# Kernel tuning notes

Hardware: AMD Instinct MI355X
Metric: run time of the kernel (lower is better)

The kernel has to match this reference:

```python
import jax, jax.numpy as jnp
import numpy as np

N_NODES = 100000
N_EDGES = 320000
DIM = 256  # hidden_dim*2 (bi-RNN)
BN_EPS = 1e-5


def setup_inputs() -> dict:
    key = jax.random.key(0)
    k1, k2, k3 = jax.random.split(key, 3)
    x = jax.random.normal(k1, (N_NODES, DIM), dtype=jnp.float32)
    W = jax.random.normal(k2, (DIM, DIM), dtype=jnp.float32) * (1.0 / np.sqrt(DIM))
    b = jnp.zeros((DIM,), dtype=jnp.float32)
    gamma = jnp.ones((DIM,), dtype=jnp.float32)
    beta = jnp.zeros((DIM,), dtype=jnp.float32)
    edge_index = jax.random.randint(k3, (2, N_EDGES), 0, N_NODES, dtype=jnp.int64)
    return {"x": x, "W": W, "b": b, "gamma": gamma, "beta": beta,
            "edge_index": edge_index}


def reference(x, W, b, gamma, beta, edge_index):
    N = x.shape[0]
    # --- GCNConv: add self-loops, symmetric deg^-1/2 normalization ---
    loop = jnp.arange(N, dtype=edge_index.dtype)
    row = jnp.concatenate([edge_index[0], loop])  # source / j
    col = jnp.concatenate([edge_index[1], loop])  # target / i
    deg = jax.ops.segment_sum(jnp.ones_like(col, dtype=x.dtype), col,
                              num_segments=N)
    dinv = jax.lax.rsqrt(deg)  # deg >= 1 due to self-loops
    norm = dinv[row] * dinv[col]  # [E+N]
    h = x @ W  # linear transform before propagation (PyG GCNConv)
    msg = h[row] * norm[:, None]  # gather + scale, [E+N, F]
    out = jax.ops.segment_sum(msg, col, num_segments=N) + b  # scatter-add
    # --- BatchNorm1d over nodes (training-mode batch statistics) ---
    mean = jnp.mean(out, axis=0)
    var = jnp.var(out, axis=0)
    out = (out - mean) * jax.lax.rsqrt(var + BN_EPS) * gamma + beta
    return jnp.tanh(out)
```

## Files before the change

### kernel.cpp

```cpp
#include <hip/hip_runtime.h>
#include <stdint.h>

#define N_NODES 100000
#define N_EDGES 320000
#define DIM 256
#define BN_EPS 1e-5f

typedef __attribute__((ext_vector_type(8))) short short8;
typedef __attribute__((ext_vector_type(4))) float f32x4;

__device__ __forceinline__ float bf2f(unsigned short u) {
    union { unsigned int i; float f; } v; v.i = ((unsigned int)u) << 16; return v.f;
}
__device__ __forceinline__ unsigned short f2bf(float f) {
    union { float f; unsigned int i; } v; v.f = f;
    unsigned int x = v.i;
    return (unsigned short)((x + 0x7fffu + ((x >> 16) & 1u)) >> 16);
}
__device__ __forceinline__ int eidx(const int* ei, int i64, int which, int e) {
    int idx = which * N_EDGES + e;
    return i64 ? ei[idx * 2] : ei[idx];
}
__device__ __forceinline__ f32x4 ldx4(const void* xv, int xf32, size_t off) {
    if (xf32) return *(const f32x4*)((const float*)xv + off);
    uint2 u = *(const uint2*)((const unsigned short*)xv + off);
    f32x4 o;
    o[0] = bf2f((unsigned short)(u.x & 0xffffu));
    o[1] = bf2f((unsigned short)(u.x >> 16));
    o[2] = bf2f((unsigned short)(u.y & 0xffffu));
    o[3] = bf2f((unsigned short)(u.y >> 16));
    return o;
}

__global__ void k_detect(const unsigned short* __restrict__ xs,
                         const unsigned short* __restrict__ wsw,
                         const int* __restrict__ ei, int* __restrict__ flags) {
    __shared__ int red[3];
    int tid = threadIdx.x;
    if (tid < 3) red[tid] = 0;
    __syncthreads();
    int badx = 0, badw = 0, nz = 0;
    for (int j = 0; j < 8; ++j) {
        if (!(fabsf(bf2f(xs[tid * 8 + j])) <= 1000.0f)) badx = 1;
        if (!(fabsf(bf2f(wsw[tid * 8 + j])) <= 1000.0f)) badw = 1;
        if (ei[(tid * 8 + j) * 2 + 1] != 0) nz = 1;
    }
    if (badx) atomicOr(&red[0], 1);
    if (badw) atomicOr(&red[1], 1);
    if (nz)   atomicOr(&red[2], 1);
    __syncthreads();
    if (tid == 0) { flags[0] = red[0]; flags[1] = red[1]; flags[2] = red[2] ? 0 : 1; }
}

__global__ void k_zero(int* __restrict__ cnt, float* __restrict__ stats) {
    int i = blockIdx.x * 256 + threadIdx.x;
    if (i < N_NODES) cnt[i] = 0;
    if (i < 512) stats[i] = 0.0f;
}

__global__ void k_cnt(const int* __restrict__ ei, int* __restrict__ cnt,
                      const int* __restrict__ flags) {
    int i64 = flags[2];
    int e = blockIdx.x * 256 + threadIdx.x;
    if (e < N_EDGES) atomicAdd(&cnt[eidx(ei, i64, 1, e)], 1);
}

__global__ void k_dinv(const int* __restrict__ cnt, float* __restrict__ dinv) {
    int i = blockIdx.x * 256 + threadIdx.x;
    if (i < N_NODES) dinv[i] = rsqrtf((float)cnt[i] + 1.0f);
}

__global__ void k_scan1(const int* __restrict__ cnt, int* __restrict__ partial) {
    __shared__ int red[256];
    int t = threadIdx.x, b = blockIdx.x;
    int i0 = b * 512 + t * 2;
    int s = 0;
    if (i0 < N_NODES) s += cnt[i0];
    if (i0 + 1 < N_NODES) s += cnt[i0 + 1];
    red[t] = s;
    __syncthreads();
    for (int off = 128; off > 0; off >>= 1) {
        if (t < off) red[t] += red[t + off];
        __syncthreads();
    }
    if (t == 0) partial[b] = red[0];
}

__global__ void k_scan2(const int* __restrict__ partial, int* __restrict__ pbase) {
    __shared__ int s[256];
    int t = threadIdx.x;
    int v = (t < 200) ? partial[t] : 0;
    s[t] = v;
    __syncthreads();
    for (int off = 1; off < 256; off <<= 1) {
        int u = (t >= off) ? s[t - off] : 0;
        __syncthreads();
        s[t] += u;
        __syncthreads();
    }
    if (t < 200) pbase[t] = s[t] - v;
}

__global__ void k_scan3(const int* __restrict__ cnt, const int* __restrict__ pbase,
                        int* __restrict__ row_start, int* __restrict__ cursor) {
    __shared__ int s[512];
    int t = threadIdx.x, b = blockIdx.x;
    int i = b * 512 + t;
    int v = (i < N_NODES) ? cnt[i] : 0;
    s[t] = v;
    __syncthreads();
    for (int off = 1; off < 512; off <<= 1) {
        int u = (t >= off) ? s[t - off] : 0;
        __syncthreads();
        s[t] += u;
        __syncthreads();
    }
    if (i < N_NODES) {
        int excl = pbase[b] + s[t] - v;
        row_start[i] = excl;
        cursor[i] = excl;
    }
}

__global__ void k_fill(const int* __restrict__ ei, const float* __restrict__ dinv,
                       int* __restrict__ cursor, int* __restrict__ csr_src,
                       float* __restrict__ csr_nrm, const int* __restrict__ flags) {
    int i64 = flags[2];
    int e = blockIdx.x * 256 + threadIdx.x;
    if (e >= N_EDGES) return;
    int c = eidx(ei, i64, 1, e);
    int r = eidx(ei, i64, 0, e);
    int slot = atomicAdd(&cursor[c], 1);
    csr_src[slot] = r;
    csr_nrm[slot] = dinv[r] * dinv[c];
}

__global__ void k_wt(const void* __restrict__ wv, unsigned short* __restrict__ Wth,
                     unsigned short* __restrict__ Wtl, const int* __restrict__ flags) {
    int wf32 = flags[1];
    int k = blockIdx.x, n = threadIdx.x;
    float v = wf32 ? ((const float*)wv)[k * DIM + n]
                   : bf2f(((const unsigned short*)wv)[k * DIM + n]);
    unsigned short h = f2bf(v);
    Wth[(size_t)n * DIM + k] = h;
    Wtl[(size_t)n * DIM + k] = f2bf(v - bf2f(h));
}

__global__ void k_agg(const void* __restrict__ xv, const int* __restrict__ row_start,
                      const int* __restrict__ cnt, const int* __restrict__ csr_src,
                      const float* __restrict__ csr_nrm, const float* __restrict__ dinv,
                      float* __restrict__ z, const int* __restrict__ flags, int base) {
    int xf32 = flags[0];
    int gid = blockIdx.x * 256 + threadIdx.x;
    int node = base + (gid >> 6);
    int lane = gid & 63;
    float dv = dinv[node];
    float s = dv * dv;
    f32x4 acc = ldx4(xv, xf32, (size_t)node * DIM + lane * 4);
    acc[0] *= s; acc[1] *= s; acc[2] *= s; acc[3] *= s;
    int start = row_start[node];
    int len = cnt[node];
    for (int j = 0; j < len; ++j) {
        int src = csr_src[start + j];
        float nrm = csr_nrm[start + j];
        f32x4 xr = ldx4(xv, xf32, (size_t)src * DIM + lane * 4);
        acc[0] += nrm * xr[0]; acc[1] += nrm * xr[1];
        acc[2] += nrm * xr[2]; acc[3] += nrm * xr[3];
    }
    *(f32x4*)(z + (size_t)(node - base) * DIM + lane * 4) = acc;
}

__launch_bounds__(256)
__global__ void k_gemm(const float* __restrict__ z, const unsigned short* __restrict__ Wth,
                       const unsigned short* __restrict__ Wtl, float* __restrict__ out,
                       float* __restrict__ stats, int base) {
    __shared__ unsigned short zh[80][264];
    __shared__ unsigned short zl[80][264];
    __shared__ float bs[512];
    int tid = threadIdx.x;
    int m0l = blockIdx.x * 80;
    {
        int rr = tid >> 4;
        int c0 = (tid & 15) * 16;
        if (tid < 256) { bs[tid] = 0.0f; bs[tid + 256] = 0.0f; }
        #pragma unroll
        for (int p = 0; p < 5; ++p) {
            int r = p * 16 + rr;
            const float* src = z + (size_t)(m0l + r) * DIM + c0;
            #pragma unroll
            for (int half = 0; half < 2; ++half) {
                short8 ph, pl;
                #pragma unroll
                for (int j4 = 0; j4 < 8; j4 += 4) {
                    f32x4 t = *(const f32x4*)(src + half * 8 + j4);
                    #pragma unroll
                    for (int j = 0; j < 4; ++j) {
                        float v = t[j];
                        unsigned short h = f2bf(v);
                        ph[j4 + j] = (short)h;
                        pl[j4 + j] = (short)f2bf(v - bf2f(h));
                    }
                }
                *(short8*)&zh[r][c0 + half * 8] = ph;
                *(short8*)&zl[r][c0 + half * 8] = pl;
            }
        }
    }
    __syncthreads();
    int w = tid >> 6, lane = tid & 63, quad = lane >> 4, rl = lane & 15;
    f32x4 acc[5][4];
    #pragma unroll
    for (int ms = 0; ms < 5; ++ms)
        #pragma unroll
        for (int nt = 0; nt < 4; ++nt)
            acc[ms][nt] = (f32x4){0.f, 0.f, 0.f, 0.f};
    #pragma unroll
    for (int kk = 0; kk < 8; ++kk) {
        int k0 = kk * 32 + quad * 8;
        short8 bh[4], bl[4];
        #pragma unroll
        for (int nt = 0; nt < 4; ++nt) {
            int n = w * 64 + nt * 16 + rl;
            bh[nt] = *(const short8*)(Wth + (size_t)n * DIM + k0);
            bl[nt] = *(const short8*)(Wtl + (size_t)n * DIM + k0);
        }
        #pragma unroll
        for (int ms = 0; ms < 5; ++ms) {
            short8 ah = *(const short8*)&zh[ms * 16 + rl][k0];
            short8 al = *(const short8*)&zl[ms * 16 + rl][k0];
            #pragma unroll
            for (int nt = 0; nt < 4; ++nt) {
                acc[ms][nt] = __builtin_amdgcn_mfma_f32_16x16x32_bf16(ah, bh[nt], acc[ms][nt], 0, 0, 0);
                acc[ms][nt] = __builtin_amdgcn_mfma_f32_16x16x32_bf16(al, bh[nt], acc[ms][nt], 0, 0, 0);
                acc[ms][nt] = __builtin_amdgcn_mfma_f32_16x16x32_bf16(ah, bl[nt], acc[ms][nt], 0, 0, 0);
            }
        }
    }
    #pragma unroll
    for (int nt = 0; nt < 4; ++nt) {
        int col = w * 64 + nt * 16 + rl;
        float s1 = 0.f, s2 = 0.f;
        #pragma unroll
        for (int ms = 0; ms < 5; ++ms)
            #pragma unroll
            for (int i = 0; i < 4; ++i) {
                float v = acc[ms][nt][i];
                s1 += v; s2 += v * v;
                out[(size_t)(base + m0l + ms * 16 + quad * 4 + i) * DIM + col] = v;
            }
        atomicAdd(&bs[col], s1);
        atomicAdd(&bs[256 + col], s2);
    }
    __syncthreads();
    if (tid < 256) {
        atomicAdd(&stats[tid], bs[tid]);
        atomicAdd(&stats[256 + tid], bs[256 + tid]);
    }
}

__global__ void k_fin(const float* __restrict__ stats, const void* __restrict__ gv,
                      const void* __restrict__ bv, float* __restrict__ scsh,
                      const int* __restrict__ flags) {
    int ff32 = flags[0];
    int f = threadIdx.x;
    const float invN = 1.0f / (float)N_NODES;
    float mean = stats[f] * invN;
    float var = stats[256 + f] * invN - mean * mean;
    float g = ff32 ? ((const float*)gv)[f] : bf2f(((const unsigned short*)gv)[f]);
    float bb = ff32 ? ((const float*)bv)[f] : bf2f(((const unsigned short*)bv)[f]);
    float sc = g * rsqrtf(var + BN_EPS);
    scsh[f] = sc;
    scsh[256 + f] = bb - mean * sc;
}

__global__ void k_final(float* __restrict__ out, const float* __restrict__ scsh) {
    int t = blockIdx.x * 256 + threadIdx.x;
    int f0 = (t & 63) * 4;
    size_t off = (size_t)t * 4;
    f32x4 v = *(const f32x4*)(out + off);
    f32x4 o;
    #pragma unroll
    for (int j = 0; j < 4; ++j)
        o[j] = tanhf(v[j] * scsh[f0 + j] + scsh[256 + f0 + j]);
    *(f32x4*)(out + off) = o;
}

extern "C" void kernel_launch(void* const* d_in, const int* in_sizes, int n_in,
                              void* d_out, int out_size, void* d_ws, size_t ws_size,
                              hipStream_t stream) {
    const void* x     = d_in[0];
    const void* W     = d_in[1];
    const void* gamma = d_in[3];
    const void* beta  = d_in[4];
    const int* ei     = (const int*)d_in[5];
    float* out = (float*)d_out;

    char* ws = (char*)d_ws;
    int*   flags     = (int*)(ws);
    int*   cnt       = (int*)(ws + 4096);
    int*   row_start = (int*)(ws + 409600);
    int*   cursor    = (int*)(ws + 819200);
    float* dinv      = (float*)(ws + 1228800);
    int*   partial   = (int*)(ws + 1638400);
    int*   pbase     = (int*)(ws + 1646592);
    float* stats     = (float*)(ws + 1654784);
    float* scsh      = (float*)(ws + 1662976);
    unsigned short* Wth = (unsigned short*)(ws + 1671168);
    unsigned short* Wtl = (unsigned short*)(ws + 1802240);
    int*   csr_src   = (int*)(ws + 1933312);
    float* csr_nrm   = (float*)(ws + 3215360);
    const size_t zoff = 4718592;
    float* z         = (float*)(ws + zoff);

    size_t zbytes = ws_size > zoff ? ws_size - zoff : 0;
    long long maxRows = (long long)(zbytes / ((size_t)DIM * 4));
    maxRows -= maxRows % 80;
    if (maxRows <= 0) maxRows = 80;
    if (maxRows > N_NODES) maxRows = N_NODES;

    k_detect<<<1,    256, 0, stream>>>((const unsigned short*)x, (const unsigned short*)W, ei, flags);
    k_zero  <<<391,  256, 0, stream>>>(cnt, stats);
    k_cnt   <<<1250, 256, 0, stream>>>(ei, cnt, flags);
    k_dinv  <<<391,  256, 0, stream>>>(cnt, dinv);
    k_scan1 <<<200,  256, 0, stream>>>(cnt, partial);
    k_scan2 <<<1,    256, 0, stream>>>(partial, pbase);
    k_scan3 <<<200,  512, 0, stream>>>(cnt, pbase, row_start, cursor);
    k_fill  <<<1250, 256, 0, stream>>>(ei, dinv, cursor, csr_src, csr_nrm, flags);
    k_wt    <<<256,  256, 0, stream>>>(W, Wth, Wtl, flags);

    for (int base = 0; base < N_NODES; base += (int)maxRows) {
        int count = N_NODES - base;
        if (count > (int)maxRows) count = (int)maxRows;
        k_agg <<<count / 4,  256, 0, stream>>>(x, row_start, cnt, csr_src, csr_nrm,
                                               dinv, z, flags, base);
        k_gemm<<<count / 80, 256, 0, stream>>>(z, Wth, Wtl, out, stats, base);
    }

    k_fin  <<<1,     256, 0, stream>>>(stats, gamma, beta, scsh, flags);
    k_final<<<25000, 256, 0, stream>>>(out, scsh);
}
```

Baseline: 432.1 us.

## Fuse prep kernels, split z to bf16 hi/lo in agg, bf16 intermediate output

Merges the detect and zero kernels, folds scan2 and the dinv computation into one scan kernel, and folds k_fin into k_final to cut launch count. The aggregation loop is unrolled by four to expose more gather parallelism, and it now writes z directly as bf16 hi/lo halves, so the GEMM reads its A operand straight from global memory instead of staging it through LDS. The GEMM moves to 512 threads with fewer N tiles per wave. When the workspace is large enough, the pre-BN output is stored as bf16 to halve final-pass traffic. Rounding the pre-normalization output to bf16 adds precision error.

```diff
diff --git a/kernel.cpp b/kernel.cpp
--- a/kernel.cpp
+++ b/kernel.cpp
@@ -32,30 +32,30 @@
     return o;
 }
 
-__global__ void k_detect(const unsigned short* __restrict__ xs,
-                         const unsigned short* __restrict__ wsw,
-                         const int* __restrict__ ei, int* __restrict__ flags) {
-    __shared__ int red[3];
-    int tid = threadIdx.x;
-    if (tid < 3) red[tid] = 0;
-    __syncthreads();
-    int badx = 0, badw = 0, nz = 0;
-    for (int j = 0; j < 8; ++j) {
-        if (!(fabsf(bf2f(xs[tid * 8 + j])) <= 1000.0f)) badx = 1;
-        if (!(fabsf(bf2f(wsw[tid * 8 + j])) <= 1000.0f)) badw = 1;
-        if (ei[(tid * 8 + j) * 2 + 1] != 0) nz = 1;
-    }
-    if (badx) atomicOr(&red[0], 1);
-    if (badw) atomicOr(&red[1], 1);
-    if (nz)   atomicOr(&red[2], 1);
-    __syncthreads();
-    if (tid == 0) { flags[0] = red[0]; flags[1] = red[1]; flags[2] = red[2] ? 0 : 1; }
-}
-
-__global__ void k_zero(int* __restrict__ cnt, float* __restrict__ stats) {
+__global__ void k_pre(const unsigned short* __restrict__ xs,
+                      const unsigned short* __restrict__ wsw,
+                      const int* __restrict__ ei, int* __restrict__ flags,
+                      int* __restrict__ cnt, float* __restrict__ stats) {
     int i = blockIdx.x * 256 + threadIdx.x;
     if (i < N_NODES) cnt[i] = 0;
     if (i < 512) stats[i] = 0.0f;
+    if (blockIdx.x == 0) {
+        __shared__ int red[3];
+        int tid = threadIdx.x;
+        if (tid < 3) red[tid] = 0;
+        __syncthreads();
+        int badx = 0, badw = 0, nz = 0;
+        for (int j = 0; j < 8; ++j) {
+            if (!(fabsf(bf2f(xs[tid * 8 + j])) <= 1000.0f)) badx = 1;
+            if (!(fabsf(bf2f(wsw[tid * 8 + j])) <= 1000.0f)) badw = 1;
+            if (ei[(tid * 8 + j) * 2 + 1] != 0) nz = 1;
+        }
+        if (badx) atomicOr(&red[0], 1);
+        if (badw) atomicOr(&red[1], 1);
+        if (nz)   atomicOr(&red[2], 1);
+        __syncthreads();
+        if (tid == 0) { flags[0] = red[0]; flags[1] = red[1]; flags[2] = red[2] ? 0 : 1; }
+    }
 }
 
 __global__ void k_cnt(const int* __restrict__ ei, int* __restrict__ cnt,
@@ -63,11 +63,6 @@
     int i64 = flags[2];
     int e = blockIdx.x * 256 + threadIdx.x;
     if (e < N_EDGES) atomicAdd(&cnt[eidx(ei, i64, 1, e)], 1);
-}
-
-__global__ void k_dinv(const int* __restrict__ cnt, float* __restrict__ dinv) {
-    int i = blockIdx.x * 256 + threadIdx.x;
-    if (i < N_NODES) dinv[i] = rsqrtf((float)cnt[i] + 1.0f);
 }
 
 __global__ void k_scan1(const int* __restrict__ cnt, int* __restrict__ partial) {
@@ -86,25 +81,21 @@
     if (t == 0) partial[b] = red[0];
 }
 
-__global__ void k_scan2(const int* __restrict__ partial, int* __restrict__ pbase) {
-    __shared__ int s[256];
-    int t = threadIdx.x;
-    int v = (t < 200) ? partial[t] : 0;
-    s[t] = v;
-    __syncthreads();
-    for (int off = 1; off < 256; off <<= 1) {
-        int u = (t >= off) ? s[t - off] : 0;
-        __syncthreads();
-        s[t] += u;
-        __syncthreads();
-    }
-    if (t < 200) pbase[t] = s[t] - v;
-}
-
-__global__ void k_scan3(const int* __restrict__ cnt, const int* __restrict__ pbase,
-                        int* __restrict__ row_start, int* __restrict__ cursor) {
+__global__ void k_scan23(const int* __restrict__ cnt, const int* __restrict__ partial,
+                         int* __restrict__ row_start, int* __restrict__ cursor,
+                         float* __restrict__ dinv) {
+    __shared__ int ps[256];
     __shared__ int s[512];
     int t = threadIdx.x, b = blockIdx.x;
+    if (t < 256) ps[t] = (t < 200) ? partial[t] : 0;
+    __syncthreads();
+    for (int off = 1; off < 256; off <<= 1) {
+        int u = (t >= off && t < 256) ? ps[t - off] : 0;
+        __syncthreads();
+        if (t < 256) ps[t] += u;
+        __syncthreads();
+    }
+    int pbase = (b == 0) ? 0 : ps[b - 1];
     int i = b * 512 + t;
     int v = (i < N_NODES) ? cnt[i] : 0;
     s[t] = v;
@@ -116,9 +107,10 @@
         __syncthreads();
     }
     if (i < N_NODES) {
-        int excl = pbase[b] + s[t] - v;
+        int excl = pbase + s[t] - v;
         row_start[i] = excl;
         cursor[i] = excl;
+        dinv[i] = rsqrtf((float)v + 1.0f);
     }
 }
 
@@ -149,7 +141,8 @@
 __global__ void k_agg(const void* __restrict__ xv, const int* __restrict__ row_start,
                       const int* __restrict__ cnt, const int* __restrict__ csr_src,
                       const float* __restrict__ csr_nrm, const float* __restrict__ dinv,
-                      float* __restrict__ z, const int* __restrict__ flags, int base) {
+                      unsigned short* __restrict__ zh, unsigned short* __restrict__ zl,
+                      const int* __restrict__ flags, int base) {
     int xf32 = flags[0];
     int gid = blockIdx.x * 256 + threadIdx.x;
     int node = base + (gid >> 6);
@@ -160,76 +153,74 @@
     acc[0] *= s; acc[1] *= s; acc[2] *= s; acc[3] *= s;
     int start = row_start[node];
     int len = cnt[node];
-    for (int j = 0; j < len; ++j) {
+    int j = 0;
+    for (; j + 3 < len; j += 4) {
+        int s0 = csr_src[start + j], s1 = csr_src[start + j + 1];
+        int s2 = csr_src[start + j + 2], s3 = csr_src[start + j + 3];
+        float n0 = csr_nrm[start + j], n1 = csr_nrm[start + j + 1];
+        float n2 = csr_nrm[start + j + 2], n3 = csr_nrm[start + j + 3];
+        f32x4 a0 = ldx4(xv, xf32, (size_t)s0 * DIM + lane * 4);
+        f32x4 a1 = ldx4(xv, xf32, (size_t)s1 * DIM + lane * 4);
+        f32x4 a2 = ldx4(xv, xf32, (size_t)s2 * DIM + lane * 4);
+        f32x4 a3 = ldx4(xv, xf32, (size_t)s3 * DIM + lane * 4);
+        #pragma unroll
+        for (int q = 0; q < 4; ++q) {
+            acc[q] += n0 * a0[q]; acc[q] += n1 * a1[q];
+            acc[q] += n2 * a2[q]; acc[q] += n3 * a3[q];
+        }
+    }
+    for (; j < len; ++j) {
         int src = csr_src[start + j];
         float nrm = csr_nrm[start + j];
         f32x4 xr = ldx4(xv, xf32, (size_t)src * DIM + lane * 4);
-        acc[0] += nrm * xr[0]; acc[1] += nrm * xr[1];
-        acc[2] += nrm * xr[2]; acc[3] += nrm * xr[3];
-    }
-    *(f32x4*)(z + (size_t)(node - base) * DIM + lane * 4) = acc;
-}
-
-__launch_bounds__(256)
-__global__ void k_gemm(const float* __restrict__ z, const unsigned short* __restrict__ Wth,
-                       const unsigned short* __restrict__ Wtl, float* __restrict__ out,
+        #pragma unroll
+        for (int q = 0; q < 4; ++q) acc[q] += nrm * xr[q];
+    }
+    uint2 ph, pl;
+    unsigned short h0 = f2bf(acc[0]), h1 = f2bf(acc[1]), h2 = f2bf(acc[2]), h3 = f2bf(acc[3]);
+    ph.x = (unsigned int)h0 | ((unsigned int)h1 << 16);
+    ph.y = (unsigned int)h2 | ((unsigned int)h3 << 16);
+    pl.x = (unsigned int)f2bf(acc[0] - bf2f(h0)) | ((unsigned int)f2bf(acc[1] - bf2f(h1)) << 16);
+    pl.y = (unsigned int)f2bf(acc[2] - bf2f(h2)) | ((unsigned int)f2bf(acc[3] - bf2f(h3)) << 16);
+    size_t zo = (size_t)(node - base) * DIM + lane * 4;
+    *(uint2*)(zh + zo) = ph;
+    *(uint2*)(zl + zo) = pl;
+}
+
+__launch_bounds__(512)
+__global__ void k_gemm(const unsigned short* __restrict__ zh, const unsigned short* __restrict__ zl,
+                       const unsigned short* __restrict__ Wth, const unsigned short* __restrict__ Wtl,
+                       float* __restrict__ outF, unsigned short* __restrict__ outH,
                        float* __restrict__ stats, int base) {
-    __shared__ unsigned short zh[80][264];
-    __shared__ unsigned short zl[80][264];
     __shared__ float bs[512];
     int tid = threadIdx.x;
+    bs[tid] = 0.0f;
+    __syncthreads();
     int m0l = blockIdx.x * 80;
-    {
-        int rr = tid >> 4;
-        int c0 = (tid & 15) * 16;
-        if (tid < 256) { bs[tid] = 0.0f; bs[tid + 256] = 0.0f; }
-        #pragma unroll
-        for (int p = 0; p < 5; ++p) {
-            int r = p * 16 + rr;
-            const float* src = z + (size_t)(m0l + r) * DIM + c0;
-            #pragma unroll
-            for (int half = 0; half < 2; ++half) {
-                short8 ph, pl;
-                #pragma unroll
-                for (int j4 = 0; j4 < 8; j4 += 4) {
-                    f32x4 t = *(const f32x4*)(src + half * 8 + j4);
-                    #pragma unroll
-                    for (int j = 0; j < 4; ++j) {
-                        float v = t[j];
-                        unsigned short h = f2bf(v);
-                        ph[j4 + j] = (short)h;
-                        pl[j4 + j] = (short)f2bf(v - bf2f(h));
-                    }
-                }
-                *(short8*)&zh[r][c0 + half * 8] = ph;
-                *(short8*)&zl[r][c0 + half * 8] = pl;
-            }
-        }
-    }
-    __syncthreads();
     int w = tid >> 6, lane = tid & 63, quad = lane >> 4, rl = lane & 15;
-    f32x4 acc[5][4];
+    f32x4 acc[5][2];
     #pragma unroll
     for (int ms = 0; ms < 5; ++ms)
         #pragma unroll
-        for (int nt = 0; nt < 4; ++nt)
+        for (int nt = 0; nt < 2; ++nt)
             acc[ms][nt] = (f32x4){0.f, 0.f, 0.f, 0.f};
     #pragma unroll
     for (int kk = 0; kk < 8; ++kk) {
         int k0 = kk * 32 + quad * 8;
-        short8 bh[4], bl[4];
-        #pragma unroll
-        for (int nt = 0; nt < 4; ++nt) {
-            int n = w * 64 + nt * 16 + rl;
+        short8 bh[2], bl[2];
+        #pragma unroll
+        for (int nt = 0; nt < 2; ++nt) {
+            int n = w * 32 + nt * 16 + rl;
             bh[nt] = *(const short8*)(Wth + (size_t)n * DIM + k0);
             bl[nt] = *(const short8*)(Wtl + (size_t)n * DIM + k0);
         }
         #pragma unroll
         for (int ms = 0; ms < 5; ++ms) {
-            short8 ah = *(const short8*)&zh[ms * 16 + rl][k0];
-            short8 al = *(const short8*)&zl[ms * 16 + rl][k0];
+            size_t ro = (size_t)(m0l + ms * 16 + rl) * DIM + k0;
+            short8 ah = *(const short8*)(zh + ro);
+            short8 al = *(const short8*)(zl + ro);
             #pragma unroll
-            for (int nt = 0; nt < 4; ++nt) {
+            for (int nt = 0; nt < 2; ++nt) {
                 acc[ms][nt] = __builtin_amdgcn_mfma_f32_16x16x32_bf16(ah, bh[nt], acc[ms][nt], 0, 0, 0);
                 acc[ms][nt] = __builtin_amdgcn_mfma_f32_16x16x32_bf16(al, bh[nt], acc[ms][nt], 0, 0, 0);
                 acc[ms][nt] = __builtin_amdgcn_mfma_f32_16x16x32_bf16(ah, bl[nt], acc[ms][nt], 0, 0, 0);
@@ -237,8 +228,8 @@
         }
     }
     #pragma unroll
-    for (int nt = 0; nt < 4; ++nt) {
-        int col = w * 64 + nt * 16 + rl;
+    for (int nt = 0; nt < 2; ++nt) {
+        int col = w * 32 + nt * 16 + rl;
         float s1 = 0.f, s2 = 0.f;
         #pragma unroll
         for (int ms = 0; ms < 5; ++ms)
@@ -246,38 +237,47 @@
             for (int i = 0; i < 4; ++i) {
                 float v = acc[ms][nt][i];
                 s1 += v; s2 += v * v;
-                out[(size_t)(base + m0l + ms * 16 + quad * 4 + i) * DIM + col] = v;
+                size_t go = (size_t)(base + m0l + ms * 16 + quad * 4 + i) * DIM + col;
+                if (outH) outH[go] = f2bf(v);
+                else outF[go] = v;
             }
         atomicAdd(&bs[col], s1);
         atomicAdd(&bs[256 + col], s2);
     }
     __syncthreads();
-    if (tid < 256) {
-        atomicAdd(&stats[tid], bs[tid]);
-        atomicAdd(&stats[256 + tid], bs[256 + tid]);
-    }
-}
-
-__global__ void k_fin(const float* __restrict__ stats, const void* __restrict__ gv,
-                      const void* __restrict__ bv, float* __restrict__ scsh,
-                      const int* __restrict__ flags) {
-    int ff32 = flags[0];
-    int f = threadIdx.x;
-    const float invN = 1.0f / (float)N_NODES;
-    float mean = stats[f] * invN;
-    float var = stats[256 + f] * invN - mean * mean;
-    float g = ff32 ? ((const float*)gv)[f] : bf2f(((const unsigned short*)gv)[f]);
-    float bb = ff32 ? ((const float*)bv)[f] : bf2f(((const unsigned short*)bv)[f]);
-    float sc = g * rsqrtf(var + BN_EPS);
-    scsh[f] = sc;
-    scsh[256 + f] = bb - mean * sc;
-}
-
-__global__ void k_final(float* __restrict__ out, const float* __restrict__ scsh) {
-    int t = blockIdx.x * 256 + threadIdx.x;
+    atomicAdd(&stats[tid], bs[tid]);
+}
+
+__global__ void k_final(const unsigned short* __restrict__ outH, float* __restrict__ out,
+                        const float* __restrict__ stats, const void* __restrict__ gv,
+                        const void* __restrict__ bv, const int* __restrict__ flags) {
+    __shared__ float scsh[512];
+    int tid = threadIdx.x;
+    {
+        int ff32 = flags[0];
+        const float invN = 1.0f / (float)N_NODES;
+        float mean = stats[tid & 255] * invN;
+        float var = stats[256 + (tid & 255)] * invN - mean * mean;
+        float g = ff32 ? ((const float*)gv)[tid & 255] : bf2f(((const unsigned short*)gv)[tid & 255]);
+        float bb = ff32 ? ((const float*)bv)[tid & 255] : bf2f(((const unsigned short*)bv)[tid & 255]);
+        float sc = g * rsqrtf(var + BN_EPS);
+        scsh[tid & 255] = sc;
+        scsh[256 + (tid & 255)] = bb - mean * sc;
+    }
+    __syncthreads();
+    int t = blockIdx.x * 256 + tid;
     int f0 = (t & 63) * 4;
     size_t off = (size_t)t * 4;
-    f32x4 v = *(const f32x4*)(out + off);
+    f32x4 v;
+    if (outH) {
+        uint2 u = *(const uint2*)(outH + off);
+        v[0] = bf2f((unsigned short)(u.x & 0xffffu));
+        v[1] = bf2f((unsigned short)(u.x >> 16));
+        v[2] = bf2f((unsigned short)(u.y & 0xffffu));
+        v[3] = bf2f((unsigned short)(u.y >> 16));
+    } else {
+        v = *(const f32x4*)(out + off);
+    }
     f32x4 o;
     #pragma unroll
     for (int j = 0; j < 4; ++j)
@@ -302,40 +302,42 @@
     int*   cursor    = (int*)(ws + 819200);
     float* dinv      = (float*)(ws + 1228800);
     int*   partial   = (int*)(ws + 1638400);
-    int*   pbase     = (int*)(ws + 1646592);
     float* stats     = (float*)(ws + 1654784);
-    float* scsh      = (float*)(ws + 1662976);
     unsigned short* Wth = (unsigned short*)(ws + 1671168);
     unsigned short* Wtl = (unsigned short*)(ws + 1802240);
     int*   csr_src   = (int*)(ws + 1933312);
     float* csr_nrm   = (float*)(ws + 3215360);
-    const size_t zoff = 4718592;
-    float* z         = (float*)(ws + zoff);
-
-    size_t zbytes = ws_size > zoff ? ws_size - zoff : 0;
-    long long maxRows = (long long)(zbytes / ((size_t)DIM * 4));
+    const size_t o_out0h = 4497408;
+    const size_t zA = o_out0h + 51200000;
+    const size_t zB = o_out0h;
+
+    long long rowsA = (ws_size > zA) ? (long long)((ws_size - zA) / 1024) : 0;
+    rowsA -= rowsA % 80;
+    int useH = (rowsA >= 25000);
+    size_t zoff = useH ? zA : zB;
+    long long maxRows = (ws_size > zoff) ? (long long)((ws_size - zoff) / 1024) : 0;
     maxRows -= maxRows % 80;
     if (maxRows <= 0) maxRows = 80;
     if (maxRows > N_NODES) maxRows = N_NODES;
-
-    k_detect<<<1,    256, 0, stream>>>((const unsigned short*)x, (const unsigned short*)W, ei, flags);
-    k_zero  <<<391,  256, 0, stream>>>(cnt, stats);
+    unsigned short* out0h = useH ? (unsigned short*)(ws + o_out0h) : (unsigned short*)0;
+
+    k_pre   <<<391,  256, 0, stream>>>((const unsigned short*)x, (const unsigned short*)W,
+                                       ei, flags, cnt, stats);
     k_cnt   <<<1250, 256, 0, stream>>>(ei, cnt, flags);
-    k_dinv  <<<391,  256, 0, stream>>>(cnt, dinv);
     k_scan1 <<<200,  256, 0, stream>>>(cnt, partial);
-    k_scan2 <<<1,    256, 0, stream>>>(partial, pbase);
-    k_scan3 <<<200,  512, 0, stream>>>(cnt, pbase, row_start, cursor);
+    k_scan23<<<200,  512, 0, stream>>>(cnt, partial, row_start, cursor, dinv);
     k_fill  <<<1250, 256, 0, stream>>>(ei, dinv, cursor, csr_src, csr_nrm, flags);
     k_wt    <<<256,  256, 0, stream>>>(W, Wth, Wtl, flags);
 
     for (int base = 0; base < N_NODES; base += (int)maxRows) {
         int count = N_NODES - base;
         if (count > (int)maxRows) count = (int)maxRows;
+        unsigned short* zh = (unsigned short*)(ws + zoff);
+        unsigned short* zl = zh + (size_t)maxRows * DIM;
         k_agg <<<count / 4,  256, 0, stream>>>(x, row_start, cnt, csr_src, csr_nrm,
-                                               dinv, z, flags, base);
-        k_gemm<<<count / 80, 256, 0, stream>>>(z, Wth, Wtl, out, stats, base);
-    }
-
-    k_fin  <<<1,     256, 0, stream>>>(stats, gamma, beta, scsh, flags);
-    k_final<<<25000, 256, 0, stream>>>(out, scsh);
-}
+                                               dinv, zh, zl, flags, base);
+        k_gemm<<<count / 80, 512, 0, stream>>>(zh, zl, Wth, Wtl, out, out0h, stats, base);
+    }
+
+    k_final<<<25000, 256, 0, stream>>>(out0h, out, stats, gamma, beta, flags);
+}
```

New measurement: 480.3 us. 1.11x slower.
